# Performance work log

Measured on AMD Instinct MI355X. Metric: run time of the kernel, lower is better.

## Reference

```python
import jax, jax.numpy as jnp
import numpy as np

VOCAB, HIDDEN, POOL, NHASH = 32000, 256, 100000, 20


def setup_inputs() -> dict:
    key = jax.random.key(0)
    k1, k2, k3, k4 = jax.random.split(key, 4)
    x = jax.random.normal(k1, (2, 2048, HIDDEN), dtype=jnp.float32)
    pool = jax.random.normal(k2, (POOL, HIDDEN), dtype=jnp.float32)
    # original init is constant 1/num_hash; use rand to make gradients nontrivial,
    # scaled similarly
    import_params = jax.random.uniform(k3, (VOCAB, NHASH), dtype=jnp.float32) / NHASH
    hash_values = jax.random.randint(k4, (VOCAB, NHASH), 0, POOL, dtype=jnp.int64)
    return {"x": x, "pool": pool, "import_params": import_params, "hash_values": hash_values}


def reference(x, pool, import_params, hash_values):
    # gather hashed embeddings: [V, J, H]
    gathered = pool[hash_values]
    # weighted sum over hashes -> [V, H]
    embed = jnp.einsum('vj,vjh->vh', import_params, gathered)
    # logits: [..., V]
    return jnp.matmul(x, embed.T)
```

## Files before the change

### kernel.cpp

```cpp
#include <hip/hip_runtime.h>
#include <hip/hip_bf16.h>

#define VOCAB  32000
#define HIDDEN 256
#define NHASH  20
#define MROWS  4096
#define KDIM   256
#define POOL   100000
#define XBLK   1024

typedef __attribute__((ext_vector_type(8))) short bf16x8;
typedef __attribute__((ext_vector_type(4))) float f32x4;

__device__ __forceinline__ unsigned short f32_bf16_rne(float f) {
  union { float f; unsigned int u; } v; v.f = f;
  unsigned int r = v.u + 0x7FFF + ((v.u >> 16) & 1);
  return (unsigned short)(r >> 16);
}

__device__ __forceinline__ float bf16_f32(unsigned short u) {
  union { unsigned int u; float f; } v; v.u = (unsigned int)u << 16;
  return v.f;
}

__device__ __forceinline__ void async16(const void* g, void* l) {
  __builtin_amdgcn_global_load_lds(
      (const __attribute__((address_space(1))) unsigned int*)g,
      (__attribute__((address_space(3))) unsigned int*)l, 16, 0, 0);
}

__device__ __forceinline__ ushort4 f4_to_bf4(float4 f) {
  ushort4 o;
  o.x = f32_bf16_rne(f.x); o.y = f32_bf16_rne(f.y);
  o.z = f32_bf16_rne(f.z); o.w = f32_bf16_rne(f.w);
  return o;
}

#define POOL_F4 (POOL * HIDDEN / 4)
#define X_F4    (MROWS * HIDDEN / 4)
__global__ __launch_bounds__(256)
void cast_kernel(const float* __restrict__ x, const float* __restrict__ pool,
                 unsigned short* __restrict__ xb, unsigned short* __restrict__ poolb) {
  const int step = gridDim.x * 256;
  for (int i = blockIdx.x * 256 + threadIdx.x; i < POOL_F4 + X_F4; i += step) {
    if (i < POOL_F4) {
      ((ushort4*)poolb)[i] = f4_to_bf4(((const float4*)pool)[i]);
    } else {
      const int j = i - POOL_F4;
      ((ushort4*)xb)[j] = f4_to_bf4(((const float4*)x)[j]);
    }
  }
}

__global__ __launch_bounds__(256)
void embed_kernel(const unsigned short* __restrict__ poolb,
                  const float* __restrict__ w, const int* __restrict__ hash,
                  unsigned short* __restrict__ eb) {
  const int v    = blockIdx.x * 4 + (threadIdx.x >> 6);
  const int lane = threadIdx.x & 63;
  int   hl = 0; float wl = 0.f;
  if (lane < NHASH) {
    hl = hash[v * NHASH + lane];
    wl = w[v * NHASH + lane];
  }
  float4 acc = make_float4(0.f, 0.f, 0.f, 0.f);
#pragma unroll
  for (int j = 0; j < NHASH; ++j) {
    const int   h  = __shfl(hl, j);
    const float ww = __shfl(wl, j);
    const ushort4 p = ((const ushort4*)(poolb + (size_t)h * HIDDEN))[lane];
    acc.x += ww * bf16_f32(p.x); acc.y += ww * bf16_f32(p.y);
    acc.z += ww * bf16_f32(p.z); acc.w += ww * bf16_f32(p.w);
  }
  ((ushort4*)(eb + (size_t)v * HIDDEN))[lane] = f4_to_bf4(acc);
}

__global__ __launch_bounds__(256)
void prep_kernel(const float* __restrict__ x, const float* __restrict__ pool,
                 const float* __restrict__ w, const int* __restrict__ hash,
                 unsigned short* __restrict__ xb, unsigned short* __restrict__ eb) {
  const int tid = threadIdx.x;
  if (blockIdx.x < XBLK) {
    const int i = blockIdx.x * 256 + tid;
    ((ushort4*)xb)[i] = f4_to_bf4(((const float4*)x)[i]);
    return;
  }
  const int v    = (blockIdx.x - XBLK) * 4 + (tid >> 6);
  const int lane = tid & 63;
  int   hl = 0; float wl = 0.f;
  if (lane < NHASH) {
    hl = hash[v * NHASH + lane];
    wl = w[v * NHASH + lane];
  }
  float4 acc = make_float4(0.f, 0.f, 0.f, 0.f);
#pragma unroll
  for (int j = 0; j < NHASH; ++j) {
    const int   h  = __shfl(hl, j);
    const float ww = __shfl(wl, j);
    const float4 p = ((const float4*)(pool + (size_t)h * HIDDEN))[lane];
    acc.x += ww * p.x; acc.y += ww * p.y;
    acc.z += ww * p.z; acc.w += ww * p.w;
  }
  ((ushort4*)(eb + (size_t)v * HIDDEN))[lane] = f4_to_bf4(acc);
}

__global__ __launch_bounds__(256)
void gemm_kernel(const unsigned short* __restrict__ xb,
                 const unsigned short* __restrict__ eb,
                 float* __restrict__ out) {
  __shared__ char smem[32768] __attribute__((aligned(128)));
  short* As = (short*)smem;
  short* Bs = (short*)(smem + 16384);
  float* Cs = (float*)smem;

  const int tid  = threadIdx.x;
  const int lane = tid & 63;
  const int wave = tid >> 6;
  const int wm   = wave >> 1;
  const int wn   = wave & 1;

  const int bid  = blockIdx.x;
  const int swz  = (bid & 7) * 1000 + (bid >> 3);
  const int mtile = swz & 31;
  const int ntile = swz >> 5;
  const int mbase = mtile * 128;
  const int nbase = ntile * 128;

  int srow[4], scol[4];
#pragma unroll
  for (int i = 0; i < 4; ++i) {
    const int c = i * 256 + tid;
    srow[i] = c >> 3;
    scol[i] = (((c & 7) ^ ((c >> 3) & 7)) << 3);
  }

  f32x4 acc[4][4] = {};

  const int abase = (wm * 64 + (lane & 15)) * 128;
  const int bbase = (wn * 64 + (lane & 15)) * 128;
  const int sw    = (lane & 7) << 4;
  const int kq    = (lane >> 4) << 4;

#pragma unroll
  for (int kt = 0; kt < 4; ++kt) {
    const int k0 = kt * 64;
#pragma unroll
    for (int i = 0; i < 4; ++i) {
      const int c = i * 256 + tid;
      async16(xb + (size_t)(mbase + srow[i]) * KDIM + k0 + scol[i], &As[c * 8]);
      async16(eb + (size_t)(nbase + srow[i]) * KDIM + k0 + scol[i], &Bs[c * 8]);
    }
    __syncthreads();

    const char* A = (const char*)As;
    const char* B = (const char*)Bs;
#pragma unroll
    for (int kk = 0; kk < 2; ++kk) {
      const int koff = (kk * 64 + kq) ^ sw;
      bf16x8 a[4], b[4];
#pragma unroll
      for (int mi = 0; mi < 4; ++mi)
        a[mi] = *(const bf16x8*)(A + abase + mi * 2048 + koff);
#pragma unroll
      for (int ni = 0; ni < 4; ++ni)
        b[ni] = *(const bf16x8*)(B + bbase + ni * 2048 + koff);
#pragma unroll
      for (int mi = 0; mi < 4; ++mi)
#pragma unroll
        for (int ni = 0; ni < 4; ++ni)
          acc[mi][ni] = __builtin_amdgcn_mfma_f32_16x16x32_bf16(
              a[mi], b[ni], acc[mi][ni], 0, 0, 0);
    }
    __syncthreads();
  }

#pragma unroll
  for (int ph = 0; ph < 2; ++ph) {
    if (wm == ph) {
      const int crow0 = (lane >> 4) << 2;
      const int ccol  = wn * 64 + (lane & 15);
#pragma unroll
      for (int mi = 0; mi < 4; ++mi)
#pragma unroll
        for (int ni = 0; ni < 4; ++ni)
#pragma unroll
          for (int j = 0; j < 4; ++j)
            Cs[(crow0 + mi * 16 + j) * 128 + ccol + ni * 16] = acc[mi][ni][j];
    }
    __syncthreads();
#pragma unroll
    for (int i = 0; i < 8; ++i) {
      const int flat = i * 1024 + tid * 4;
      const int row  = flat >> 7;
      const int col  = flat & 127;
      f32x4 vv = *(const f32x4*)&Cs[row * 128 + col];
      __builtin_nontemporal_store(vv,
          (f32x4*)&out[(size_t)(mbase + ph * 64 + row) * VOCAB + nbase + col]);
    }
    if (ph == 0) __syncthreads();
  }
}

extern "C" void kernel_launch(void* const* d_in, const int* in_sizes, int n_in,
                              void* d_out, int out_size, void* d_ws, size_t ws_size,
                              hipStream_t stream) {
  const float* x    = (const float*)d_in[0];
  const float* pool = (const float*)d_in[1];
  const float* imp  = (const float*)d_in[2];
  const int*   hash = (const int*)d_in[3];
  float* out = (float*)d_out;

  unsigned short* xb    = (unsigned short*)d_ws;
  unsigned short* eb    = xb + (size_t)MROWS * HIDDEN;
  unsigned short* poolb = eb + (size_t)VOCAB * HIDDEN;

  const size_t need = ((size_t)MROWS + VOCAB + POOL) * HIDDEN * 2;
  if (ws_size >= need) {
    cast_kernel<<<2048, 256, 0, stream>>>(x, pool, xb, poolb);
    embed_kernel<<<VOCAB / 4, 256, 0, stream>>>(poolb, imp, hash, eb);
  } else {
    prep_kernel<<<XBLK + VOCAB / 4, 256, 0, stream>>>(x, pool, imp, hash, xb, eb);
  }
  gemm_kernel<<<(MROWS / 128) * (VOCAB / 128), 256, 0, stream>>>(xb, eb, out);
}
```

Measured before the change: 190.1 us.

## Fuse embedding gather into GEMM with persistent N-tile blocks holding B in LDS

The separate embed kernel and GEMM are merged. Each of 500 blocks computes a 128-row slice of the hashed embedding directly into swizzled LDS, then loops over 16 M tiles while reusing that resident B tile. Only A is streamed per tile. This removes the intermediate embedding write/read and a launch. In exchange it uses only 500 blocks with 80KB LDS each, so occupancy and parallelism drop, and A loading is no longer overlapped with compute.

```diff
diff --git a/kernel.cpp b/kernel.cpp
--- a/kernel.cpp
+++ b/kernel.cpp
@@ -7,7 +7,6 @@
 #define MROWS  4096
 #define KDIM   256
 #define POOL   100000
-#define XBLK   1024
 
 typedef __attribute__((ext_vector_type(8))) short bf16x8;
 typedef __attribute__((ext_vector_type(4))) float f32x4;
@@ -53,65 +52,22 @@
 }
 
 __global__ __launch_bounds__(256)
-void embed_kernel(const unsigned short* __restrict__ poolb,
+void xcast_kernel(const float* __restrict__ x, unsigned short* __restrict__ xb) {
+  const int i = blockIdx.x * 256 + threadIdx.x;
+  ((ushort4*)xb)[i] = f4_to_bf4(((const float4*)x)[i]);
+}
+
+template <bool BF16POOL>
+__global__ __launch_bounds__(256)
+void fused_kernel(const unsigned short* __restrict__ poolb,
+                  const float* __restrict__ poolf,
                   const float* __restrict__ w, const int* __restrict__ hash,
-                  unsigned short* __restrict__ eb) {
-  const int v    = blockIdx.x * 4 + (threadIdx.x >> 6);
-  const int lane = threadIdx.x & 63;
-  int   hl = 0; float wl = 0.f;
-  if (lane < NHASH) {
-    hl = hash[v * NHASH + lane];
-    wl = w[v * NHASH + lane];
-  }
-  float4 acc = make_float4(0.f, 0.f, 0.f, 0.f);
-#pragma unroll
-  for (int j = 0; j < NHASH; ++j) {
-    const int   h  = __shfl(hl, j);
-    const float ww = __shfl(wl, j);
-    const ushort4 p = ((const ushort4*)(poolb + (size_t)h * HIDDEN))[lane];
-    acc.x += ww * bf16_f32(p.x); acc.y += ww * bf16_f32(p.y);
-    acc.z += ww * bf16_f32(p.z); acc.w += ww * bf16_f32(p.w);
-  }
-  ((ushort4*)(eb + (size_t)v * HIDDEN))[lane] = f4_to_bf4(acc);
-}
-
-__global__ __launch_bounds__(256)
-void prep_kernel(const float* __restrict__ x, const float* __restrict__ pool,
-                 const float* __restrict__ w, const int* __restrict__ hash,
-                 unsigned short* __restrict__ xb, unsigned short* __restrict__ eb) {
-  const int tid = threadIdx.x;
-  if (blockIdx.x < XBLK) {
-    const int i = blockIdx.x * 256 + tid;
-    ((ushort4*)xb)[i] = f4_to_bf4(((const float4*)x)[i]);
-    return;
-  }
-  const int v    = (blockIdx.x - XBLK) * 4 + (tid >> 6);
-  const int lane = tid & 63;
-  int   hl = 0; float wl = 0.f;
-  if (lane < NHASH) {
-    hl = hash[v * NHASH + lane];
-    wl = w[v * NHASH + lane];
-  }
-  float4 acc = make_float4(0.f, 0.f, 0.f, 0.f);
-#pragma unroll
-  for (int j = 0; j < NHASH; ++j) {
-    const int   h  = __shfl(hl, j);
-    const float ww = __shfl(wl, j);
-    const float4 p = ((const float4*)(pool + (size_t)h * HIDDEN))[lane];
-    acc.x += ww * p.x; acc.y += ww * p.y;
-    acc.z += ww * p.z; acc.w += ww * p.w;
-  }
-  ((ushort4*)(eb + (size_t)v * HIDDEN))[lane] = f4_to_bf4(acc);
-}
-
-__global__ __launch_bounds__(256)
-void gemm_kernel(const unsigned short* __restrict__ xb,
-                 const unsigned short* __restrict__ eb,
-                 float* __restrict__ out) {
-  __shared__ char smem[32768] __attribute__((aligned(128)));
-  short* As = (short*)smem;
-  short* Bs = (short*)(smem + 16384);
-  float* Cs = (float*)smem;
+                  const unsigned short* __restrict__ xb,
+                  float* __restrict__ out) {
+  __shared__ char smem[81920] __attribute__((aligned(128)));
+  char*  Bp   = smem;
+  short* Abuf = (short*)(smem + 65536);
+  float* Cs   = (float*)(smem + 65536);
 
   const int tid  = threadIdx.x;
   const int lane = tid & 63;
@@ -119,12 +75,37 @@
   const int wm   = wave >> 1;
   const int wn   = wave & 1;
 
-  const int bid  = blockIdx.x;
-  const int swz  = (bid & 7) * 1000 + (bid >> 3);
-  const int mtile = swz & 31;
-  const int ntile = swz >> 5;
-  const int mbase = mtile * 128;
+  const int ntile = blockIdx.x >> 1;
+  const int mhalf = blockIdx.x & 1;
   const int nbase = ntile * 128;
+
+#pragma unroll 1
+  for (int r = 0; r < 32; ++r) {
+    const int row = wave * 32 + r;
+    const int v   = nbase + row;
+    int hl = 0; float wl = 0.f;
+    if (lane < NHASH) {
+      hl = hash[v * NHASH + lane];
+      wl = w[v * NHASH + lane];
+    }
+    float4 a4 = make_float4(0.f, 0.f, 0.f, 0.f);
+#pragma unroll
+    for (int j = 0; j < NHASH; ++j) {
+      const int   h  = __shfl(hl, j);
+      const float ww = __shfl(wl, j);
+      if (BF16POOL) {
+        const ushort4 p = ((const ushort4*)(poolb + (size_t)h * HIDDEN))[lane];
+        a4.x += ww * bf16_f32(p.x); a4.y += ww * bf16_f32(p.y);
+        a4.z += ww * bf16_f32(p.z); a4.w += ww * bf16_f32(p.w);
+      } else {
+        const float4 p = ((const float4*)(poolf + (size_t)h * HIDDEN))[lane];
+        a4.x += ww * p.x; a4.y += ww * p.y;
+        a4.z += ww * p.z; a4.w += ww * p.w;
+      }
+    }
+    *(ushort4*)(Bp + row * 512 + ((lane * 8) ^ ((row & 7) << 4))) = f4_to_bf4(a4);
+  }
+  __syncthreads();
 
   int srow[4], scol[4];
 #pragma unroll
@@ -134,70 +115,75 @@
     scol[i] = (((c & 7) ^ ((c >> 3) & 7)) << 3);
   }
 
-  f32x4 acc[4][4] = {};
-
   const int abase = (wm * 64 + (lane & 15)) * 128;
-  const int bbase = (wn * 64 + (lane & 15)) * 128;
+  const int brow  = wn * 64 + (lane & 15);
   const int sw    = (lane & 7) << 4;
   const int kq    = (lane >> 4) << 4;
 
-#pragma unroll
-  for (int kt = 0; kt < 4; ++kt) {
-    const int k0 = kt * 64;
-#pragma unroll
-    for (int i = 0; i < 4; ++i) {
-      const int c = i * 256 + tid;
-      async16(xb + (size_t)(mbase + srow[i]) * KDIM + k0 + scol[i], &As[c * 8]);
-      async16(eb + (size_t)(nbase + srow[i]) * KDIM + k0 + scol[i], &Bs[c * 8]);
-    }
-    __syncthreads();
-
-    const char* A = (const char*)As;
-    const char* B = (const char*)Bs;
-#pragma unroll
-    for (int kk = 0; kk < 2; ++kk) {
-      const int koff = (kk * 64 + kq) ^ sw;
-      bf16x8 a[4], b[4];
-#pragma unroll
-      for (int mi = 0; mi < 4; ++mi)
-        a[mi] = *(const bf16x8*)(A + abase + mi * 2048 + koff);
-#pragma unroll
-      for (int ni = 0; ni < 4; ++ni)
-        b[ni] = *(const bf16x8*)(B + bbase + ni * 2048 + koff);
-#pragma unroll
-      for (int mi = 0; mi < 4; ++mi)
+#pragma unroll 1
+  for (int mt = 0; mt < 16; ++mt) {
+    const int mbase = (mhalf * 16 + mt) * 128;
+    f32x4 acc[4][4] = {};
+
+#pragma unroll
+    for (int kt = 0; kt < 4; ++kt) {
+      const int k0 = kt * 64;
+#pragma unroll
+      for (int i = 0; i < 4; ++i) {
+        const int c = i * 256 + tid;
+        async16(xb + (size_t)(mbase + srow[i]) * KDIM + k0 + scol[i], &Abuf[c * 8]);
+      }
+      __syncthreads();
+
+      const char* A = (const char*)Abuf;
+#pragma unroll
+      for (int kk = 0; kk < 2; ++kk) {
+        const int koffA = (kk * 64 + kq) ^ sw;
+        const int koffB = ((kt * 128 + kk * 64 + kq) ^ sw);
+        bf16x8 a[4], b[4];
+#pragma unroll
+        for (int mi = 0; mi < 4; ++mi)
+          a[mi] = *(const bf16x8*)(A + abase + mi * 2048 + koffA);
 #pragma unroll
         for (int ni = 0; ni < 4; ++ni)
-          acc[mi][ni] = __builtin_amdgcn_mfma_f32_16x16x32_bf16(
-              a[mi], b[ni], acc[mi][ni], 0, 0, 0);
-    }
-    __syncthreads();
-  }
-
-#pragma unroll
-  for (int ph = 0; ph < 2; ++ph) {
-    if (wm == ph) {
-      const int crow0 = (lane >> 4) << 2;
-      const int ccol  = wn * 64 + (lane & 15);
-#pragma unroll
-      for (int mi = 0; mi < 4; ++mi)
-#pragma unroll
-        for (int ni = 0; ni < 4; ++ni)
-#pragma unroll
-          for (int j = 0; j < 4; ++j)
-            Cs[(crow0 + mi * 16 + j) * 128 + ccol + ni * 16] = acc[mi][ni][j];
-    }
-    __syncthreads();
-#pragma unroll
-    for (int i = 0; i < 8; ++i) {
-      const int flat = i * 1024 + tid * 4;
-      const int row  = flat >> 7;
-      const int col  = flat & 127;
-      f32x4 vv = *(const f32x4*)&Cs[row * 128 + col];
-      __builtin_nontemporal_store(vv,
-          (f32x4*)&out[(size_t)(mbase + ph * 64 + row) * VOCAB + nbase + col]);
-    }
-    if (ph == 0) __syncthreads();
+          b[ni] = *(const bf16x8*)(Bp + (brow + ni * 16) * 512 + koffB);
+#pragma unroll
+        for (int mi = 0; mi < 4; ++mi)
+#pragma unroll
+          for (int ni = 0; ni < 4; ++ni)
+            acc[mi][ni] = __builtin_amdgcn_mfma_f32_16x16x32_bf16(
+                a[mi], b[ni], acc[mi][ni], 0, 0, 0);
+      }
+      __syncthreads();
+    }
+
+#pragma unroll
+    for (int p = 0; p < 4; ++p) {
+      if (wm == (p >> 1)) {
+        const int r0 = ((lane >> 4) << 2);
+        const int c0 = wn * 64 + (lane & 15);
+#pragma unroll
+        for (int q = 0; q < 2; ++q) {
+          const int mi = (p & 1) * 2 + q;
+#pragma unroll
+          for (int ni = 0; ni < 4; ++ni)
+#pragma unroll
+            for (int j = 0; j < 4; ++j)
+              Cs[(q * 16 + r0 + j) * 128 + c0 + ni * 16] = acc[mi][ni][j];
+        }
+      }
+      __syncthreads();
+#pragma unroll
+      for (int i = 0; i < 4; ++i) {
+        const int flat = i * 1024 + tid * 4;
+        const int row  = flat >> 7;
+        const int col  = flat & 127;
+        f32x4 vv = *(const f32x4*)&Cs[row * 128 + col];
+        __builtin_nontemporal_store(vv,
+            (f32x4*)&out[(size_t)(mbase + p * 32 + row) * VOCAB + nbase + col]);
+      }
+      __syncthreads();
+    }
   }
 }
 
@@ -211,15 +197,14 @@
   float* out = (float*)d_out;
 
   unsigned short* xb    = (unsigned short*)d_ws;
-  unsigned short* eb    = xb + (size_t)MROWS * HIDDEN;
-  unsigned short* poolb = eb + (size_t)VOCAB * HIDDEN;
-
-  const size_t need = ((size_t)MROWS + VOCAB + POOL) * HIDDEN * 2;
+  unsigned short* poolb = xb + (size_t)MROWS * HIDDEN;
+
+  const size_t need = ((size_t)MROWS + POOL) * HIDDEN * 2;
   if (ws_size >= need) {
     cast_kernel<<<2048, 256, 0, stream>>>(x, pool, xb, poolb);
-    embed_kernel<<<VOCAB / 4, 256, 0, stream>>>(poolb, imp, hash, eb);
+    fused_kernel<true><<<500, 256, 0, stream>>>(poolb, nullptr, imp, hash, xb, out);
   } else {
-    prep_kernel<<<XBLK + VOCAB / 4, 256, 0, stream>>>(x, pool, imp, hash, xb, eb);
-  }
-  gemm_kernel<<<(MROWS / 128) * (VOCAB / 128), 256, 0, stream>>>(xb, eb, out);
-}
+    xcast_kernel<<<X_F4 / 256, 256, 0, stream>>>(x, xb);
+    fused_kernel<false><<<500, 256, 0, stream>>>(nullptr, pool, imp, hash, xb, out);
+  }
+}
```

New measurement: 210.6 us. 1.11x slower.
